# Optimization experiments

Hardware: AMD Instinct MI355X
Metric: run time of the kernel (lower is better)

Reference implementation:

```python
import jax, jax.numpy as jnp
import numpy as np

B, S, H, DH = 2, 2048, 24, 32
E = H * DH  # 768


def setup_inputs() -> dict:
    key = jax.random.key(0)
    ks = jax.random.split(key, 7)
    embedding = jax.random.normal(ks[0], (B, S, E), dtype=jnp.float32)
    mask = jax.random.randint(ks[1], (B, S, S), 0, 2).astype(bool)
    # per-head QKV weights (applied as x @ W, equivalent param to torch Linear W.T)
    Wq = jax.random.normal(ks[2], (H, DH, DH), dtype=jnp.float32) * 0.05
    Wk = jax.random.normal(ks[3], (H, DH, DH), dtype=jnp.float32) * 0.05
    Wv = jax.random.normal(ks[4], (H, DH, DH), dtype=jnp.float32) * 0.05
    Wo = jax.random.normal(ks[5], (E, E), dtype=jnp.float32) * 0.02
    bo = jax.random.normal(ks[6], (E,), dtype=jnp.float32) * 0.02
    return {"embedding": embedding, "mask": mask, "Wq": Wq, "Wk": Wk,
            "Wv": Wv, "Wo": Wo, "bo": bo}


def reference(embedding, mask, Wq, Wk, Wv, Wo, bo):
    # split channels into heads: [B,S,H,DH]
    xh = embedding.reshape(B, S, H, DH)
    # per-head projections (batched over heads)
    Q = jnp.einsum('bshd,hde->bhse', xh, Wq)
    K = jnp.einsum('bshd,hde->bhse', xh, Wk)
    V = jnp.einsum('bshd,hde->bhse', xh, Wv)
    scale = 1.0 / jnp.sqrt(jnp.float32(DH))
    scores = jnp.einsum('bhqd,bhkd->bhqk', Q, K) * scale
    # faithful quirk: masked positions set to -1e-6 (not -inf)
    scores = jnp.where(mask[:, None, :, :], scores, jnp.float32(-1e-6))
    probs = jax.nn.softmax(scores, axis=-1)
    out = jnp.einsum('bhqk,bhkd->bqhd', probs, V)  # [B,S,H,DH]
    out = out.reshape(B, S, E)  # concat heads along feature dim
    return out @ Wo.T + bo
```

## Files before the change

### kernel.cpp

```cpp
#include <hip/hip_runtime.h>
#include <hip/hip_bf16.h>

#define B_  2
#define S_  2048
#define H_  24
#define DH_ 32
#define E_  768
#define SW_ (S_/32)

#define NB_MASK ((B_*S_*S_)/256)
#define NB_WO   ((E_*E_)/1024)
#define NB_WT   (H_)

typedef __attribute__((ext_vector_type(8))) short short8;
typedef __attribute__((ext_vector_type(4))) float f32x4;

static __device__ __forceinline__ float bf16tof(short s) {
    unsigned u = ((unsigned)(unsigned short)s) << 16;
    return __builtin_bit_cast(float, u);
}
static __device__ __forceinline__ short4 pack4(float a, float b, float c, float d) {
    union { __hip_bfloat162 h[2]; short4 s; } u;
    u.h[0] = __float22bfloat162_rn(make_float2(a, b));
    u.h[1] = __float22bfloat162_rn(make_float2(c, d));
    return u.s;
}
static __device__ __forceinline__ short8 pack8f(const float* a, const float* b) {
    union { __hip_bfloat162 h[4]; short8 s; } u;
    u.h[0] = __float22bfloat162_rn(make_float2(a[0], a[1]));
    u.h[1] = __float22bfloat162_rn(make_float2(a[2], a[3]));
    u.h[2] = __float22bfloat162_rn(make_float2(b[0], b[1]));
    u.h[3] = __float22bfloat162_rn(make_float2(b[2], b[3]));
    return u.s;
}
static __device__ __forceinline__ short8 pack8(float4 a, float4 b) {
    union { __hip_bfloat162 h[4]; short8 s; } u;
    u.h[0] = __float22bfloat162_rn(make_float2(a.x, a.y));
    u.h[1] = __float22bfloat162_rn(make_float2(a.z, a.w));
    u.h[2] = __float22bfloat162_rn(make_float2(b.x, b.y));
    u.h[3] = __float22bfloat162_rn(make_float2(b.z, b.w));
    return u.s;
}

#define QSCALE  0.25503487f
#define MEXP    0.99999899864f

__global__ __launch_bounds__(256) void prep_kernel(
    const int* __restrict__ mask, const float* __restrict__ Wo,
    const float* __restrict__ Wq, const float* __restrict__ Wk,
    const float* __restrict__ Wv,
    unsigned int* __restrict__ mbits, __hip_bfloat16* __restrict__ Wob,
    __hip_bfloat16* __restrict__ WTq, __hip_bfloat16* __restrict__ WTk,
    __hip_bfloat16* __restrict__ WTv)
{
    const int bx = blockIdx.x;
    if (bx < NB_MASK) {
        const int idx  = bx * 256 + threadIdx.x;
        const int lane = threadIdx.x & 63;
        const unsigned long long bal = __ballot(mask[idx] != 0);
        if (lane == 0) {
            uint2 w;
            w.x = (unsigned int)(bal & 0xffffffffull);
            w.y = (unsigned int)(bal >> 32);
            *reinterpret_cast<uint2*>(mbits + (idx >> 5)) = w;
        }
    } else if (bx < NB_MASK + NB_WO) {
        const int i = ((bx - NB_MASK) * 256 + threadIdx.x) * 4;
        const float4 w = *reinterpret_cast<const float4*>(Wo + i);
        *reinterpret_cast<short4*>(Wob + i) = pack4(w.x, w.y, w.z, w.w);
    } else {
        const int h = bx - NB_MASK - NB_WO;
        const int base = h * DH_ * DH_;
        for (int i = threadIdx.x; i < DH_ * DH_; i += 256) {
            const int d = i >> 5, e = i & 31;
            WTq[base + e * 32 + d] = __float2bfloat16(Wq[base + i]);
            WTk[base + e * 32 + d] = __float2bfloat16(Wk[base + i]);
            WTv[base + e * 32 + d] = __float2bfloat16(Wv[base + i]);
        }
    }
}

__global__ __launch_bounds__(256) void qkv_kernel(
    const float* __restrict__ x,
    const __hip_bfloat16* __restrict__ WTq,
    const __hip_bfloat16* __restrict__ WTk,
    const __hip_bfloat16* __restrict__ WTv,
    __hip_bfloat16* __restrict__ Qo,
    __hip_bfloat16* __restrict__ Ko,
    __hip_bfloat16* __restrict__ Vto)
{
    const int bh   = blockIdx.y;
    const int b    = bh / H_;
    const int h    = bh - b * H_;
    const int wave = threadIdx.x >> 6;
    const int lane = threadIdx.x & 63;
    const int col  = lane & 15;
    const int quad = lane >> 4;
    const int sw   = blockIdx.x * 64 + wave * 16;
    const int s    = sw + col;

    const float* xp = x + ((size_t)b * S_ + s) * E_ + h * DH_ + quad * 8;
    const float4 xa = *reinterpret_cast<const float4*>(xp);
    const float4 xb = *reinterpret_cast<const float4*>(xp + 4);
    const short8 xf = pack8(xa, xb);

    const int wofs = h * DH_ * DH_ + col * 32 + quad * 8;
    const short8 aQ0 = *reinterpret_cast<const short8*>(WTq + wofs);
    const short8 aQ1 = *reinterpret_cast<const short8*>(WTq + wofs + 16 * 32);
    const short8 aK0 = *reinterpret_cast<const short8*>(WTk + wofs);
    const short8 aK1 = *reinterpret_cast<const short8*>(WTk + wofs + 16 * 32);
    const short8 bV0 = *reinterpret_cast<const short8*>(WTv + wofs);
    const short8 bV1 = *reinterpret_cast<const short8*>(WTv + wofs + 16 * 32);

    const f32x4 z = {0.f, 0.f, 0.f, 0.f};
    const f32x4 qt0 = __builtin_amdgcn_mfma_f32_16x16x32_bf16(aQ0, xf, z, 0, 0, 0);
    const f32x4 qt1 = __builtin_amdgcn_mfma_f32_16x16x32_bf16(aQ1, xf, z, 0, 0, 0);
    const f32x4 kt0 = __builtin_amdgcn_mfma_f32_16x16x32_bf16(aK0, xf, z, 0, 0, 0);
    const f32x4 kt1 = __builtin_amdgcn_mfma_f32_16x16x32_bf16(aK1, xf, z, 0, 0, 0);
    const f32x4 vv0 = __builtin_amdgcn_mfma_f32_16x16x32_bf16(xf, bV0, z, 0, 0, 0);
    const f32x4 vv1 = __builtin_amdgcn_mfma_f32_16x16x32_bf16(xf, bV1, z, 0, 0, 0);

    __hip_bfloat16* qrow = Qo + ((size_t)bh * S_ + s) * DH_;
    *reinterpret_cast<short4*>(qrow + quad * 4) =
        pack4(qt0[0] * QSCALE, qt0[1] * QSCALE, qt0[2] * QSCALE, qt0[3] * QSCALE);
    *reinterpret_cast<short4*>(qrow + 16 + quad * 4) =
        pack4(qt1[0] * QSCALE, qt1[1] * QSCALE, qt1[2] * QSCALE, qt1[3] * QSCALE);

    const int t32  = s & 31;
    const int slot = (s & ~31) | (((t32 >> 2) & 1) << 4)
                   | (((t32 >> 3) << 2) | (t32 & 3));
    __hip_bfloat16* krow = Ko + ((size_t)bh * S_ + slot) * DH_;
    *reinterpret_cast<short4*>(krow + quad * 4)      = pack4(kt0[0], kt0[1], kt0[2], kt0[3]);
    *reinterpret_cast<short4*>(krow + 16 + quad * 4) = pack4(kt1[0], kt1[1], kt1[2], kt1[3]);

    const int sb = sw + quad * 4;
    *reinterpret_cast<short4*>(Vto + ((size_t)bh * DH_ + col) * S_ + sb) =
        pack4(vv0[0], vv0[1], vv0[2], vv0[3]);
    *reinterpret_cast<short4*>(Vto + ((size_t)bh * DH_ + 16 + col) * S_ + sb) =
        pack4(vv1[0], vv1[1], vv1[2], vv1[3]);
}

__global__ __launch_bounds__(256) void attn_kernel(
    const __hip_bfloat16* __restrict__ Q,
    const __hip_bfloat16* __restrict__ K,
    const __hip_bfloat16* __restrict__ Vt,
    const unsigned int* __restrict__ mbits,
    __hip_bfloat16* __restrict__ Opart,
    float* __restrict__ lpart)
{
    const int bh   = blockIdx.y;
    const int b    = bh / H_;
    const int h    = bh - b * H_;
    const int part = blockIdx.z;
    const int niter = (S_ / 32) / gridDim.z;
    const int kbeg = part * niter * 32;
    const int wave = threadIdx.x >> 6;
    const int lane = threadIdx.x & 63;
    const int col  = lane & 15;
    const int quad = lane >> 4;
    const int q0   = blockIdx.x * 256 + wave * 64;

    const __hip_bfloat16* Qbh = Q  + (size_t)bh * S_ * DH_;
    const __hip_bfloat16* Kbh = K  + (size_t)bh * S_ * DH_;
    const __hip_bfloat16* Vbh = Vt + (size_t)bh * DH_ * S_;

    short8 qf[4];
#pragma unroll
    for (int t = 0; t < 4; ++t)
        qf[t] = *reinterpret_cast<const short8*>(
            Qbh + (size_t)(q0 + t * 16 + col) * DH_ + quad * 8);

    const __hip_bfloat16* Kp  = Kbh + (size_t)(kbeg + col) * DH_ + quad * 8;
    const __hip_bfloat16* Vp0 = Vbh + (size_t)col * S_ + kbeg + quad * 8;
    const __hip_bfloat16* Vp1 = Vbh + (size_t)(16 + col) * S_ + kbeg + quad * 8;
    const unsigned int* mbb = mbits + (size_t)b * S_ * SW_ + (kbeg >> 5);
    const unsigned int* mp[4];
#pragma unroll
    for (int t = 0; t < 4; ++t)
        mp[t] = mbb + (size_t)(q0 + t * 16 + col) * SW_;

    f32x4 o0a[4], o1a[4];
    float la[4];
#pragma unroll
    for (int t = 0; t < 4; ++t) {
        o0a[t] = (f32x4){0.f,0.f,0.f,0.f};
        o1a[t] = (f32x4){0.f,0.f,0.f,0.f};
        la[t]  = 0.f;
    }

    for (int it = 0; it < niter; ++it) {
        unsigned int mw[4];
#pragma unroll
        for (int t = 0; t < 4; ++t) mw[t] = *mp[t];

        const short8 kf0 = *reinterpret_cast<const short8*>(Kp);
        const short8 kf1 = *reinterpret_cast<const short8*>(Kp + 16 * DH_);
        const short8 vf0 = *reinterpret_cast<const short8*>(Vp0);
        const short8 vf1 = *reinterpret_cast<const short8*>(Vp1);

        const f32x4 z = {0.f, 0.f, 0.f, 0.f};
        f32x4 s0[4], s1[4];
#pragma unroll
        for (int t = 0; t < 4; ++t) {
            s0[t] = __builtin_amdgcn_mfma_f32_16x16x32_bf16(kf0, qf[t], z, 0, 0, 0);
            s1[t] = __builtin_amdgcn_mfma_f32_16x16x32_bf16(kf1, qf[t], z, 0, 0, 0);
        }

#pragma unroll
        for (int t = 0; t < 4; ++t) {
            float p0[4], p1[4];
#pragma unroll
            for (int r = 0; r < 4; ++r) {
                const int kb = quad * 8 + r;
                const float e0 = __builtin_amdgcn_exp2f(s0[t][r]);
                const float e1 = __builtin_amdgcn_exp2f(s1[t][r]);
                p0[r] = ((mw[t] >> kb)       & 1u) ? e0 : MEXP;
                p1[r] = ((mw[t] >> (kb + 4)) & 1u) ? e1 : MEXP;
            }
            la[t] += ((p0[0] + p0[1]) + (p0[2] + p0[3]))
                   + ((p1[0] + p1[1]) + (p1[2] + p1[3]));
            const short8 pf = pack8f(p0, p1);
            o0a[t] = __builtin_amdgcn_mfma_f32_16x16x32_bf16(vf0, pf, o0a[t], 0, 0, 0);
            o1a[t] = __builtin_amdgcn_mfma_f32_16x16x32_bf16(vf1, pf, o1a[t], 0, 0, 0);
        }

        Kp  += 32 * DH_;
        Vp0 += 32;
        Vp1 += 32;
#pragma unroll
        for (int t = 0; t < 4; ++t) mp[t] += 1;
    }

    __hip_bfloat16* Ob = Opart + (size_t)part * B_ * S_ * E_;
    float* lp = lpart + (size_t)part * B_ * H_ * S_ + (size_t)bh * S_;
#pragma unroll
    for (int t = 0; t < 4; ++t) {
        float l = la[t];
        l += __shfl_xor(l, 16);
        l += __shfl_xor(l, 32);
        __hip_bfloat16* orow = Ob + ((size_t)b * S_ + q0 + t * 16 + col) * E_ + h * DH_;
        *reinterpret_cast<short4*>(orow + quad * 4) =
            pack4(o0a[t][0], o0a[t][1], o0a[t][2], o0a[t][3]);
        *reinterpret_cast<short4*>(orow + 16 + quad * 4) =
            pack4(o1a[t][0], o1a[t][1], o1a[t][2], o1a[t][3]);
        if (quad == 0) lp[q0 + t * 16 + col] = l;
    }
}

template <int PARTS>
__global__ __launch_bounds__(256) void proj_kernel(
    const __hip_bfloat16* __restrict__ Opart,
    const float* __restrict__ lpart,
    const __hip_bfloat16* __restrict__ Wob,
    const float* __restrict__ bo,
    float* __restrict__ out)
{
    const int wave = threadIdx.x >> 6;
    const int lane = threadIdx.x & 63;
    const int col  = lane & 15;
    const int quad = lane >> 4;
    const int m0   = blockIdx.x * 16;
    const int n0   = blockIdx.y * 256 + wave * 64;

    const int m = m0 + col;
    const int b = m / S_;
    const int s = m - b * S_;
    const float* lpb = lpart + (size_t)(b * H_) * S_ + s;

    f32x4 acc[4] = {{0.f,0.f,0.f,0.f},{0.f,0.f,0.f,0.f},
                    {0.f,0.f,0.f,0.f},{0.f,0.f,0.f,0.f}};
    for (int k0 = 0; k0 < E_; k0 += 32) {
        const int h = k0 >> 5;
        const size_t aofs = (size_t)m * E_ + k0 + quad * 8;
        float av[8] = {0.f,0.f,0.f,0.f,0.f,0.f,0.f,0.f};
        float l = 0.f;
#pragma unroll
        for (int pp = 0; pp < PARTS; ++pp) {
            const short8 a = *reinterpret_cast<const short8*>(
                Opart + (size_t)pp * B_ * S_ * E_ + aofs);
            l += lpb[(size_t)pp * B_ * H_ * S_ + (size_t)h * S_];
#pragma unroll
            for (int i = 0; i < 8; ++i) av[i] += bf16tof(a[i]);
        }
        const float linv = 1.0f / l;
#pragma unroll
        for (int i = 0; i < 8; ++i) av[i] *= linv;
        const short8 af = pack8f(av, av + 4);

#pragma unroll
        for (int j = 0; j < 4; ++j) {
            const short8 bf = *reinterpret_cast<const short8*>(
                Wob + (size_t)(n0 + j * 16 + col) * E_ + k0 + quad * 8);
            acc[j] = __builtin_amdgcn_mfma_f32_16x16x32_bf16(af, bf, acc[j], 0, 0, 0);
        }
    }
#pragma unroll
    for (int j = 0; j < 4; ++j) {
        const int n = n0 + j * 16 + col;
        const float bias = bo[n];
#pragma unroll
        for (int r = 0; r < 4; ++r) {
            const int mm = m0 + quad * 4 + r;
            out[(size_t)mm * E_ + n] = acc[j][r] + bias;
        }
    }
}

extern "C" void kernel_launch(void* const* d_in, const int* in_sizes, int n_in,
                              void* d_out, int out_size, void* d_ws, size_t ws_size,
                              hipStream_t stream)
{
    const float* emb = (const float*)d_in[0];
    const int*   msk = (const int*)d_in[1];
    const float* Wq  = (const float*)d_in[2];
    const float* Wk  = (const float*)d_in[3];
    const float* Wv  = (const float*)d_in[4];
    const float* Wo  = (const float*)d_in[5];
    const float* bo  = (const float*)d_in[6];
    float* out = (float*)d_out;

    const size_t nqkv = (size_t)B_ * H_ * S_ * DH_;
    char* p = (char*)d_ws;
    __hip_bfloat16* Q    = (__hip_bfloat16*)p;  p += nqkv * 2;
    __hip_bfloat16* Kp   = (__hip_bfloat16*)p;  p += nqkv * 2;
    __hip_bfloat16* Vt   = (__hip_bfloat16*)p;  p += nqkv * 2;
    unsigned int*  mbits = (unsigned int*)p;    p += (size_t)B_ * S_ * SW_ * 4;
    __hip_bfloat16* Wob  = (__hip_bfloat16*)p;  p += (size_t)E_ * E_ * 2;
    __hip_bfloat16* WTq  = (__hip_bfloat16*)p;  p += (size_t)H_ * DH_ * DH_ * 2;
    __hip_bfloat16* WTk  = (__hip_bfloat16*)p;  p += (size_t)H_ * DH_ * DH_ * 2;
    __hip_bfloat16* WTv  = (__hip_bfloat16*)p;  p += (size_t)H_ * DH_ * DH_ * 2;
    __hip_bfloat16* Op   = (__hip_bfloat16*)p;
    const size_t base = (size_t)(p - (char*)d_ws);

    int parts = 1;
    {
        const size_t need = base + (size_t)2 * nqkv * 2
                          + (size_t)2 * B_ * H_ * S_ * 4;
        if (ws_size >= need) parts = 2;
    }
    float* lpart = (float*)(Op + (size_t)parts * nqkv);

    prep_kernel<<<NB_MASK + NB_WO + NB_WT, 256, 0, stream>>>(
        msk, Wo, Wq, Wk, Wv, mbits, Wob, WTq, WTk, WTv);
    qkv_kernel <<<dim3(S_ / 64, B_ * H_), 256, 0, stream>>>(
        emb, WTq, WTk, WTv, Q, Kp, Vt);
    attn_kernel<<<dim3(S_ / 256, B_ * H_, parts), 256, 0, stream>>>(
        Q, Kp, Vt, mbits, Op, lpart);
    if (parts == 2)
        proj_kernel<2><<<dim3((B_ * S_) / 16, E_ / 256), 256, 0, stream>>>(
            Op, lpart, Wob, bo, out);
    else
        proj_kernel<1><<<dim3((B_ * S_) / 16, E_ / 256), 256, 0, stream>>>(
            Op, lpart, Wob, bo, out);
}
```

Baseline: 247.3 us.

## Unroll attention loop by two key tiles, use MFMA for row sums, remap blocks per XCD

The attention loop now handles 64 keys per iteration. It loads two sets of K/V fragments and a 64-bit mask word up front so more memory traffic is in flight at once. The softmax denominator is now accumulated with an extra MFMA against a vector of ones, replacing the scalar adds and the cross-lane shuffles. The grid is flattened to 1D and remapped so each XCD works on a fixed set of (batch, head) pairs, aiming for better L2 locality of K/V and the mask. The costs are higher register pressure, an extra MFMA per tile, and row sums built from bf16-rounded probabilities.

```diff
diff --git a/kernel.cpp b/kernel.cpp
--- a/kernel.cpp
+++ b/kernel.cpp
@@ -146,19 +146,26 @@
     const __hip_bfloat16* __restrict__ Vt,
     const unsigned int* __restrict__ mbits,
     __hip_bfloat16* __restrict__ Opart,
-    float* __restrict__ lpart)
-{
-    const int bh   = blockIdx.y;
+    float* __restrict__ lpart,
+    int parts)
+{
+    const int bid  = blockIdx.x;
+    const int xcd  = bid & 7;
+    const int t_   = bid >> 3;
+    const int bh   = xcd * 6 + (t_ % 6);
+    const int rest = t_ / 6;
+    const int qblk = rest & 7;
+    const int part = rest >> 3;
+
     const int b    = bh / H_;
     const int h    = bh - b * H_;
-    const int part = blockIdx.z;
-    const int niter = (S_ / 32) / gridDim.z;
-    const int kbeg = part * niter * 32;
+    const int niter = S_ / (64 * parts);
+    const int kbeg  = part * (S_ / parts);
     const int wave = threadIdx.x >> 6;
     const int lane = threadIdx.x & 63;
     const int col  = lane & 15;
     const int quad = lane >> 4;
-    const int q0   = blockIdx.x * 256 + wave * 64;
+    const int q0   = qblk * 256 + wave * 64;
 
     const __hip_bfloat16* Qbh = Q  + (size_t)bh * S_ * DH_;
     const __hip_bfloat16* Kbh = K  + (size_t)bh * S_ * DH_;
@@ -179,33 +186,40 @@
     for (int t = 0; t < 4; ++t)
         mp[t] = mbb + (size_t)(q0 + t * 16 + col) * SW_;
 
-    f32x4 o0a[4], o1a[4];
-    float la[4];
+    const short ONE = 0x3F80;
+    const short8 ones = {ONE, ONE, ONE, ONE, ONE, ONE, ONE, ONE};
+
+    f32x4 o0a[4], o1a[4], la[4];
 #pragma unroll
     for (int t = 0; t < 4; ++t) {
         o0a[t] = (f32x4){0.f,0.f,0.f,0.f};
         o1a[t] = (f32x4){0.f,0.f,0.f,0.f};
-        la[t]  = 0.f;
+        la[t]  = (f32x4){0.f,0.f,0.f,0.f};
     }
 
     for (int it = 0; it < niter; ++it) {
-        unsigned int mw[4];
-#pragma unroll
-        for (int t = 0; t < 4; ++t) mw[t] = *mp[t];
-
-        const short8 kf0 = *reinterpret_cast<const short8*>(Kp);
-        const short8 kf1 = *reinterpret_cast<const short8*>(Kp + 16 * DH_);
-        const short8 vf0 = *reinterpret_cast<const short8*>(Vp0);
-        const short8 vf1 = *reinterpret_cast<const short8*>(Vp1);
+        uint2 mw[4];
+#pragma unroll
+        for (int t = 0; t < 4; ++t)
+            mw[t] = *reinterpret_cast<const uint2*>(mp[t]);
+
+        const short8 kA0 = *reinterpret_cast<const short8*>(Kp);
+        const short8 kA1 = *reinterpret_cast<const short8*>(Kp + 16 * DH_);
+        const short8 vA0 = *reinterpret_cast<const short8*>(Vp0);
+        const short8 vA1 = *reinterpret_cast<const short8*>(Vp1);
+        const short8 kB0 = *reinterpret_cast<const short8*>(Kp + 32 * DH_);
+        const short8 kB1 = *reinterpret_cast<const short8*>(Kp + 48 * DH_);
+        const short8 vB0 = *reinterpret_cast<const short8*>(Vp0 + 32);
+        const short8 vB1 = *reinterpret_cast<const short8*>(Vp1 + 32);
 
         const f32x4 z = {0.f, 0.f, 0.f, 0.f};
+
         f32x4 s0[4], s1[4];
 #pragma unroll
         for (int t = 0; t < 4; ++t) {
-            s0[t] = __builtin_amdgcn_mfma_f32_16x16x32_bf16(kf0, qf[t], z, 0, 0, 0);
-            s1[t] = __builtin_amdgcn_mfma_f32_16x16x32_bf16(kf1, qf[t], z, 0, 0, 0);
-        }
-
+            s0[t] = __builtin_amdgcn_mfma_f32_16x16x32_bf16(kA0, qf[t], z, 0, 0, 0);
+            s1[t] = __builtin_amdgcn_mfma_f32_16x16x32_bf16(kA1, qf[t], z, 0, 0, 0);
+        }
 #pragma unroll
         for (int t = 0; t < 4; ++t) {
             float p0[4], p1[4];
@@ -214,36 +228,54 @@
                 const int kb = quad * 8 + r;
                 const float e0 = __builtin_amdgcn_exp2f(s0[t][r]);
                 const float e1 = __builtin_amdgcn_exp2f(s1[t][r]);
-                p0[r] = ((mw[t] >> kb)       & 1u) ? e0 : MEXP;
-                p1[r] = ((mw[t] >> (kb + 4)) & 1u) ? e1 : MEXP;
+                p0[r] = ((mw[t].x >> kb)       & 1u) ? e0 : MEXP;
+                p1[r] = ((mw[t].x >> (kb + 4)) & 1u) ? e1 : MEXP;
             }
-            la[t] += ((p0[0] + p0[1]) + (p0[2] + p0[3]))
-                   + ((p1[0] + p1[1]) + (p1[2] + p1[3]));
             const short8 pf = pack8f(p0, p1);
-            o0a[t] = __builtin_amdgcn_mfma_f32_16x16x32_bf16(vf0, pf, o0a[t], 0, 0, 0);
-            o1a[t] = __builtin_amdgcn_mfma_f32_16x16x32_bf16(vf1, pf, o1a[t], 0, 0, 0);
-        }
-
-        Kp  += 32 * DH_;
-        Vp0 += 32;
-        Vp1 += 32;
-#pragma unroll
-        for (int t = 0; t < 4; ++t) mp[t] += 1;
+            o0a[t] = __builtin_amdgcn_mfma_f32_16x16x32_bf16(vA0, pf, o0a[t], 0, 0, 0);
+            o1a[t] = __builtin_amdgcn_mfma_f32_16x16x32_bf16(vA1, pf, o1a[t], 0, 0, 0);
+            la[t]  = __builtin_amdgcn_mfma_f32_16x16x32_bf16(ones, pf, la[t], 0, 0, 0);
+        }
+
+#pragma unroll
+        for (int t = 0; t < 4; ++t) {
+            s0[t] = __builtin_amdgcn_mfma_f32_16x16x32_bf16(kB0, qf[t], z, 0, 0, 0);
+            s1[t] = __builtin_amdgcn_mfma_f32_16x16x32_bf16(kB1, qf[t], z, 0, 0, 0);
+        }
+#pragma unroll
+        for (int t = 0; t < 4; ++t) {
+            float p0[4], p1[4];
+#pragma unroll
+            for (int r = 0; r < 4; ++r) {
+                const int kb = quad * 8 + r;
+                const float e0 = __builtin_amdgcn_exp2f(s0[t][r]);
+                const float e1 = __builtin_amdgcn_exp2f(s1[t][r]);
+                p0[r] = ((mw[t].y >> kb)       & 1u) ? e0 : MEXP;
+                p1[r] = ((mw[t].y >> (kb + 4)) & 1u) ? e1 : MEXP;
+            }
+            const short8 pf = pack8f(p0, p1);
+            o0a[t] = __builtin_amdgcn_mfma_f32_16x16x32_bf16(vB0, pf, o0a[t], 0, 0, 0);
+            o1a[t] = __builtin_amdgcn_mfma_f32_16x16x32_bf16(vB1, pf, o1a[t], 0, 0, 0);
+            la[t]  = __builtin_amdgcn_mfma_f32_16x16x32_bf16(ones, pf, la[t], 0, 0, 0);
+        }
+
+        Kp  += 64 * DH_;
+        Vp0 += 64;
+        Vp1 += 64;
+#pragma unroll
+        for (int t = 0; t < 4; ++t) mp[t] += 2;
     }
 
     __hip_bfloat16* Ob = Opart + (size_t)part * B_ * S_ * E_;
     float* lp = lpart + (size_t)part * B_ * H_ * S_ + (size_t)bh * S_;
 #pragma unroll
     for (int t = 0; t < 4; ++t) {
-        float l = la[t];
-        l += __shfl_xor(l, 16);
-        l += __shfl_xor(l, 32);
         __hip_bfloat16* orow = Ob + ((size_t)b * S_ + q0 + t * 16 + col) * E_ + h * DH_;
         *reinterpret_cast<short4*>(orow + quad * 4) =
             pack4(o0a[t][0], o0a[t][1], o0a[t][2], o0a[t][3]);
         *reinterpret_cast<short4*>(orow + 16 + quad * 4) =
             pack4(o1a[t][0], o1a[t][1], o1a[t][2], o1a[t][3]);
-        if (quad == 0) lp[q0 + t * 16 + col] = l;
+        if (quad == 0) lp[q0 + t * 16 + col] = la[t][0];
     }
 }
 
@@ -344,8 +376,8 @@
         msk, Wo, Wq, Wk, Wv, mbits, Wob, WTq, WTk, WTv);
     qkv_kernel <<<dim3(S_ / 64, B_ * H_), 256, 0, stream>>>(
         emb, WTq, WTk, WTv, Q, Kp, Vt);
-    attn_kernel<<<dim3(S_ / 256, B_ * H_, parts), 256, 0, stream>>>(
-        Q, Kp, Vt, mbits, Op, lpart);
+    attn_kernel<<<384 * parts, 256, 0, stream>>>(
+        Q, Kp, Vt, mbits, Op, lpart, parts);
     if (parts == 2)
         proj_kernel<2><<<dim3((B_ * S_) / 16, E_ / 256), 256, 0, stream>>>(
             Op, lpart, Wob, bo, out);
```

Result: faster. 233.5 us (-5.6%).
